# Kernel optimization log

Hardware: AMD Instinct MI355X
Metric: run time of the kernel (lower is better)

The kernel has to match this reference:

```python
import jax, jax.numpy as jnp
import numpy as np

NEG_INF_MASK = -10000.0


def setup_inputs() -> dict:
    key = jax.random.key(0)
    ks = jax.random.split(key, 6)
    B, S, D, H, K = 2, 2048, 1024, 16, 64
    return {
        "from_tensor": jax.random.normal(ks[0], (B, S, D), jnp.float32),
        "to_tensor": jax.random.normal(ks[1], (B, S, D), jnp.float32),
        "attention_mask": jax.random.randint(ks[2], (B, S), 0, 2, jnp.int32),
        "Wq": jax.random.normal(ks[3], (D, H, K), jnp.float32) * 0.02,
        "bq": jnp.zeros((H, K), jnp.float32),
        "Wk": jax.random.normal(ks[4], (D, H, K), jnp.float32) * 0.02,
        "bk": jnp.zeros((H, K), jnp.float32),
        "Wv": jax.random.normal(ks[5], (D, H, K), jnp.float32) * 0.02,
        "bv": jnp.zeros((H, K), jnp.float32),
    }


def reference(from_tensor, to_tensor, attention_mask, Wq, bq, Wk, bk, Wv, bv):
    # 3D dense projections: [B,S,D] x [D,H,K] -> [B,H,S,K] (transpose fused into einsum)
    q = jnp.einsum("bfd,dhk->bhfk", from_tensor, Wq) + bq[None, :, None, :]
    k = jnp.einsum("btd,dhk->bhtk", to_tensor, Wk) + bk[None, :, None, :]
    v = jnp.einsum("btd,dhk->bhtk", to_tensor, Wv) + bv[None, :, None, :]

    head_dim = q.shape[-1]
    logits = jnp.einsum("bhfk,bhtk->bhft", q, k) / jnp.sqrt(jnp.float32(head_dim))

    # key-padding mask: ones[B,1,F,1] @ mask[B,1,T,1]^T == broadcast mask over F
    mask = attention_mask.astype(jnp.float32)[:, None, None, :]  # [B,1,1,T]
    logits = logits + (1.0 - mask) * NEG_INF_MASK

    probs = jax.nn.softmax(logits, axis=-1)  # dropout prob = 0.0 -> no-op
    # context: [B,H,F,T] x [B,H,T,K] -> [B,F,H,K] (output transpose fused)
    return jnp.einsum("bhft,bhtk->bfhk", probs, v)
```

## Files before the change

kernel.cpp:

```cpp
#include <hip/hip_runtime.h>
#include <hip/hip_bf16.h>
#include <stdint.h>

#define B_   2
#define S_   2048
#define D_   1024
#define H_   16
#define KD_  64
#define TB   64

typedef __bf16 bf16_t;
typedef __bf16 bf16x8 __attribute__((ext_vector_type(8)));
typedef __bf16 bf16x4 __attribute__((ext_vector_type(4)));
typedef float  f32x4  __attribute__((ext_vector_type(4)));

#define MFMA16(A, B, C) __builtin_amdgcn_mfma_f32_16x16x32_bf16((A), (B), (C), 0, 0, 0)

__device__ __forceinline__ void gload_lds16(const void* g, void* l) {
    auto gp = (const __attribute__((address_space(1))) void*)(uintptr_t)(g);
    auto lp = (__attribute__((address_space(3))) void*)(uint32_t)(uintptr_t)(l);
    __builtin_amdgcn_global_load_lds(gp, lp, 16, 0, 0);
}

__global__ __launch_bounds__(256) void cvt_f32_bf16(const float* __restrict__ in,
                                                    bf16_t* __restrict__ out, int n4) {
    int idx = blockIdx.x * blockDim.x + threadIdx.x;
    int stride = gridDim.x * blockDim.x;
    for (int i = idx; i < n4; i += stride) {
        float4 v = ((const float4*)in)[i];
        bf16x4 o = {(bf16_t)v.x, (bf16_t)v.y, (bf16_t)v.z, (bf16_t)v.w};
        ((bf16x4*)out)[i] = o;
    }
}

__global__ __launch_bounds__(256) void transpose_w(const float* __restrict__ W,
                                                   bf16_t* __restrict__ Wt) {
    __shared__ float tile[32][33];
    const int tx = threadIdx.x & 31;
    const int ty = threadIdx.x >> 5;
    const int bx = blockIdx.x * 32;
    const int by = blockIdx.y * 32;
#pragma unroll
    for (int j = 0; j < 32; j += 8)
        tile[ty + j][tx] = W[(size_t)(by + ty + j) * D_ + bx + tx];
    __syncthreads();
#pragma unroll
    for (int j = 0; j < 32; j += 8)
        Wt[(size_t)(bx + ty + j) * D_ + by + tx] = (bf16_t)tile[tx][ty + j];
}

__global__ __launch_bounds__(256) void mask_k(const int* __restrict__ mask,
                                              float* __restrict__ madd, int n) {
    int i = blockIdx.x * blockDim.x + threadIdx.x;
    if (i < n) madd[i] = (1.0f - (float)mask[i]) * -10000.0f;
}

__global__ __launch_bounds__(512) void proj_gemm_fused(const bf16_t* __restrict__ Xf,
                                                       const bf16_t* __restrict__ Xt,
                                                       const bf16_t* __restrict__ Wt0,
                                                       const float* __restrict__ bq,
                                                       const float* __restrict__ bk,
                                                       const float* __restrict__ bv,
                                                       bf16_t* __restrict__ Qb,
                                                       bf16_t* __restrict__ Kb,
                                                       bf16_t* __restrict__ Vtb) {
    __shared__ bf16_t As[128 * 32];
    __shared__ bf16_t Bs[128 * 32];
    const int which = blockIdx.z;
    const bf16_t* X  = (which == 0) ? Xf : Xt;
    const bf16_t* Wt = Wt0 + (size_t)which * D_ * D_;
    const float* bias = (which == 0) ? bq : (which == 1) ? bk : bv;

    const int tid  = threadIdx.x;
    const int w    = tid >> 6;
    const int lane = tid & 63;
    const int wr   = w >> 2;
    const int wc   = w & 3;
    const int g    = lane >> 4;
    const int c    = lane & 15;
    const int m0 = blockIdx.y * 128;
    const int n0 = blockIdx.x * 128;

    f32x4 acc[4][2] = {};

    const int srow = w * 16 + (lane >> 2);
    const int scol = (lane & 3) * 8;
    const bf16_t* gA = X  + (size_t)(m0 + srow) * D_ + scol;
    const bf16_t* gB = Wt + (size_t)(n0 + srow) * D_ + scol;
    char* lA = (char*)As + w * 1024;
    char* lB = (char*)Bs + w * 1024;

    for (int k0 = 0; k0 < D_; k0 += 32) {
        __syncthreads();
        gload_lds16(gA + k0, lA);
        gload_lds16(gB + k0, lB);
        __syncthreads();

        bf16x8 af[4], bfr[2];
#pragma unroll
        for (int i = 0; i < 4; ++i)
            af[i] = *(const bf16x8*)&As[(wr * 64 + i * 16 + c) * 32 + g * 8];
#pragma unroll
        for (int j = 0; j < 2; ++j)
            bfr[j] = *(const bf16x8*)&Bs[(wc * 32 + j * 16 + c) * 32 + g * 8];
#pragma unroll
        for (int i = 0; i < 4; ++i)
#pragma unroll
            for (int j = 0; j < 2; ++j)
                acc[i][j] = MFMA16(af[i], bfr[j], acc[i][j]);
    }

#pragma unroll
    for (int i = 0; i < 4; ++i)
#pragma unroll
        for (int j = 0; j < 2; ++j)
#pragma unroll
            for (int r = 0; r < 4; ++r) {
                int m = m0 + wr * 64 + i * 16 + g * 4 + r;
                int n = n0 + wc * 32 + j * 16 + c;
                float val = acc[i][j][r] + bias[n];
                int b = m >> 11, s = m & 2047, hh = n >> 6, kd = n & 63;
                if (which == 0)
                    Qb[(size_t)(((b * H_ + hh) * S_ + s)) * KD_ + kd] = (bf16_t)(val * 0.125f);
                else if (which == 1)
                    Kb[(size_t)(((b * H_ + hh) * S_ + s)) * KD_ + kd] = (bf16_t)val;
                else
                    Vtb[(size_t)(((b * H_ + hh) * KD_ + kd)) * S_ + s] = (bf16_t)val;
            }
}

__global__ __launch_bounds__(256) void attn_kernel(const bf16_t* __restrict__ Q,
                                                   const bf16_t* __restrict__ K,
                                                   const bf16_t* __restrict__ Vt,
                                                   const float* __restrict__ maskadd,
                                                   float* __restrict__ out) {
    __shared__ __align__(16) bf16_t Ks[2][8 * 64 * 8];
    __shared__ __align__(16) bf16_t Vs[2][8 * 64 * 8];
    __shared__ __align__(16) float  Ms[S_];
    __shared__ __align__(16) bf16_t P_lds[4][32][88];
    const int tid = threadIdx.x;
    const int w = tid >> 6, lane = tid & 63;
    const int g = lane >> 4, c = lane & 15;
    const int b = blockIdx.z, h = blockIdx.y;
    const int qbase = blockIdx.x * 128 + w * 32;

    const bf16_t* Qp = Q + (size_t)(b * H_ + h) * S_ * KD_;
    const char* Kb8 = (const char*)(K + (size_t)(b * H_ + h) * S_ * KD_);
    const char* Vb8 = (const char*)(Vt + (size_t)(b * H_ + h) * KD_ * S_);
    const float* mp = maskadd + b * S_;

    {
        const float4* src = (const float4*)mp;
        float4* dst = (float4*)Ms;
        dst[tid] = src[tid];
        dst[tid + 256] = src[tid + 256];
    }

    bf16x8 qf[2][2];
#pragma unroll
    for (int qh = 0; qh < 2; ++qh) {
        qf[qh][0] = *(const bf16x8*)&Qp[(size_t)(qbase + qh * 16 + c) * KD_ + g * 8];
        qf[qh][1] = *(const bf16x8*)&Qp[(size_t)(qbase + qh * 16 + c) * KD_ + 32 + g * 8];
    }

    const char* srcK = Kb8 + lane * 128 + w * 16;
    const char* srcV = Vb8 + (size_t)lane * (S_ * 2) + w * 16;

    f32x4 o_acc[2][4] = {};
    float l_part[2][4] = {};

    {
        char* dK = (char*)Ks + w * 1024;
        char* dV = (char*)Vs + w * 1024;
        gload_lds16(srcK, dK);
        gload_lds16(srcK + 64, dK + 4096);
        gload_lds16(srcV, dV);
        gload_lds16(srcV + 64, dV + 4096);
    }
    __syncthreads();

    int buf = 0;
    for (int t0 = 0; t0 < S_; t0 += TB) {
        if (t0 + TB < S_) {
            char* dK = (char*)Ks + (buf ^ 1) * 8192 + w * 1024;
            char* dV = (char*)Vs + (buf ^ 1) * 8192 + w * 1024;
            gload_lds16(srcK + (t0 + TB) * 128,      dK);
            gload_lds16(srcK + (t0 + TB) * 128 + 64, dK + 4096);
            gload_lds16(srcV + (t0 + TB) * 2,        dV);
            gload_lds16(srcV + (t0 + TB) * 2 + 64,   dV + 4096);
        }
        const char* ksb = (const char*)Ks + buf * 8192;
        const char* vsb = (const char*)Vs + buf * 8192;

        f32x4 s[2][4];
#pragma unroll
        for (int tc = 0; tc < 4; ++tc) {
            const int row = tc * 16 + c;
            bf16x8 k0 = *(const bf16x8*)(ksb + g * 1024 + row * 16);
            bf16x8 k1 = *(const bf16x8*)(ksb + (4 + g) * 1024 + row * 16);
#pragma unroll
            for (int qh = 0; qh < 2; ++qh) {
                f32x4 z = {};
                z = MFMA16(qf[qh][0], k0, z);
                s[qh][tc] = MFMA16(qf[qh][1], k1, z);
            }
        }
#pragma unroll
        for (int tc = 0; tc < 4; ++tc) {
            float ma = Ms[t0 + tc * 16 + c];
#pragma unroll
            for (int qh = 0; qh < 2; ++qh)
#pragma unroll
                for (int r = 0; r < 4; ++r) s[qh][tc][r] += ma;
        }
#pragma unroll
        for (int qh = 0; qh < 2; ++qh) {
#pragma unroll
            for (int r = 0; r < 4; ++r) {
                float rs = 0.f;
#pragma unroll
                for (int tc = 0; tc < 4; ++tc) {
                    float p = __expf(s[qh][tc][r]);
                    s[qh][tc][r] = p;
                    rs += p;
                }
                l_part[qh][r] += rs;
            }
#pragma unroll
            for (int tc = 0; tc < 4; ++tc)
#pragma unroll
                for (int r = 0; r < 4; ++r)
                    P_lds[w][qh * 16 + g * 4 + r][tc * 16 + c] = (bf16_t)s[qh][tc][r];
        }
        bf16x8 pa[2][2];
#pragma unroll
        for (int qh = 0; qh < 2; ++qh) {
            pa[qh][0] = *(const bf16x8*)&P_lds[w][qh * 16 + c][g * 8];
            pa[qh][1] = *(const bf16x8*)&P_lds[w][qh * 16 + c][32 + g * 8];
        }
#pragma unroll
        for (int nc = 0; nc < 4; ++nc) {
            const int row = nc * 16 + c;
            bf16x8 v0 = *(const bf16x8*)(vsb + g * 1024 + row * 16);
            bf16x8 v1 = *(const bf16x8*)(vsb + (4 + g) * 1024 + row * 16);
#pragma unroll
            for (int qh = 0; qh < 2; ++qh) {
                o_acc[qh][nc] = MFMA16(pa[qh][0], v0, o_acc[qh][nc]);
                o_acc[qh][nc] = MFMA16(pa[qh][1], v1, o_acc[qh][nc]);
            }
        }
        __syncthreads();
        buf ^= 1;
    }
#pragma unroll
    for (int qh = 0; qh < 2; ++qh)
#pragma unroll
        for (int r = 0; r < 4; ++r) {
            float rs = l_part[qh][r];
            rs += __shfl_xor(rs, 1);
            rs += __shfl_xor(rs, 2);
            rs += __shfl_xor(rs, 4);
            rs += __shfl_xor(rs, 8);
            l_part[qh][r] = rs;
        }
#pragma unroll
    for (int qh = 0; qh < 2; ++qh)
#pragma unroll
        for (int nc = 0; nc < 4; ++nc)
#pragma unroll
            for (int r = 0; r < 4; ++r) {
                int qrow = qbase + qh * 16 + g * 4 + r;
                out[(size_t)((b * S_ + qrow) * H_ + h) * KD_ + nc * 16 + c] =
                    o_acc[qh][nc][r] / l_part[qh][r];
            }
}

extern "C" void kernel_launch(void* const* d_in, const int* in_sizes, int n_in,
                              void* d_out, int out_size, void* d_ws, size_t ws_size,
                              hipStream_t stream) {
    const float* from = (const float*)d_in[0];
    const float* to   = (const float*)d_in[1];
    const int*   amsk = (const int*)d_in[2];
    const float* Wq   = (const float*)d_in[3];
    const float* bq   = (const float*)d_in[4];
    const float* Wk   = (const float*)d_in[5];
    const float* bk   = (const float*)d_in[6];
    const float* Wv   = (const float*)d_in[7];
    const float* bv   = (const float*)d_in[8];
    float* out = (float*)d_out;
    char* ws = (char*)d_ws;

    const size_t SZ_X   = (size_t)(B_ * S_) * D_ * 2;
    const size_t SZ_W   = (size_t)D_ * D_ * 2;
    const size_t SZ_QKV = (size_t)B_ * H_ * S_ * KD_ * 2;
    size_t off = 0;
    bf16_t* Xf  = (bf16_t*)(ws + off); off += SZ_X;
    bf16_t* Xt  = (bf16_t*)(ws + off); off += SZ_X;
    bf16_t* Wtq = (bf16_t*)(ws + off); off += SZ_W;
    bf16_t* Wtk = (bf16_t*)(ws + off); off += SZ_W;
    bf16_t* Wtv = (bf16_t*)(ws + off); off += SZ_W;
    bf16_t* Qb  = (bf16_t*)(ws + off); off += SZ_QKV;
    bf16_t* Kb  = (bf16_t*)(ws + off); off += SZ_QKV;
    bf16_t* Vtb = (bf16_t*)(ws + off); off += SZ_QKV;
    float*  madd = (float*)(ws + off); off += (size_t)B_ * S_ * 4;

    const int n4 = (B_ * S_ * D_) / 4;
    cvt_f32_bf16<<<2048, 256, 0, stream>>>(from, Xf, n4);
    cvt_f32_bf16<<<2048, 256, 0, stream>>>(to,   Xt, n4);
    transpose_w<<<dim3(32, 32), 256, 0, stream>>>(Wq, Wtq);
    transpose_w<<<dim3(32, 32), 256, 0, stream>>>(Wk, Wtk);
    transpose_w<<<dim3(32, 32), 256, 0, stream>>>(Wv, Wtv);
    mask_k<<<(B_ * S_ + 255) / 256, 256, 0, stream>>>(amsk, madd, B_ * S_);

    proj_gemm_fused<<<dim3(D_ / 128, (B_ * S_) / 128, 3), 512, 0, stream>>>(
        Xf, Xt, Wtq, bq, bk, bv, Qb, Kb, Vtb);

    attn_kernel<<<dim3(S_ / 128, H_, B_), 256, 0, stream>>>(Qb, Kb, Vtb, madd, out);
}
```

Baseline: 208.0 us.

## Merge prep launches, fold mask into attention, double-buffer projection GEMM LDS

The two f32-to-bf16 conversions become one launch using grid z, and the three weight transposes become one launch. The separate mask kernel is removed and the additive mask is computed from the int mask directly inside the attention kernel's LDS fill. The projection GEMM now double-buffers its A/B LDS tiles, prefetching the next k-slice with global_load_lds while computing the current one, so one barrier per iteration is removed. This cuts launch overhead and aims to overlap load latency with MFMA work. The cost is twice the LDS in the GEMM. The prefetch is issued without an explicit wait before the barrier, so correctness relies on the barrier covering completion of the async LDS loads.

```diff
diff --git a/kernel.cpp b/kernel.cpp
--- a/kernel.cpp
+++ b/kernel.cpp
@@ -22,8 +22,12 @@
     __builtin_amdgcn_global_load_lds(gp, lp, 16, 0, 0);
 }
 
-__global__ __launch_bounds__(256) void cvt_f32_bf16(const float* __restrict__ in,
-                                                    bf16_t* __restrict__ out, int n4) {
+__global__ __launch_bounds__(256) void cvt_f32_bf16_2(const float* __restrict__ a,
+                                                      const float* __restrict__ bt,
+                                                      bf16_t* __restrict__ oa,
+                                                      bf16_t* __restrict__ ob, int n4) {
+    const float* in = blockIdx.z ? bt : a;
+    bf16_t* out = blockIdx.z ? ob : oa;
     int idx = blockIdx.x * blockDim.x + threadIdx.x;
     int stride = gridDim.x * blockDim.x;
     for (int i = idx; i < n4; i += stride) {
@@ -33,8 +37,13 @@
     }
 }
 
-__global__ __launch_bounds__(256) void transpose_w(const float* __restrict__ W,
-                                                   bf16_t* __restrict__ Wt) {
+__global__ __launch_bounds__(256) void transpose_w3(const float* __restrict__ Wq,
+                                                    const float* __restrict__ Wk,
+                                                    const float* __restrict__ Wv,
+                                                    bf16_t* __restrict__ Wt0) {
+    const int z = blockIdx.z;
+    const float* W = (z == 0) ? Wq : (z == 1) ? Wk : Wv;
+    bf16_t* Wt = Wt0 + (size_t)z * D_ * D_;
     __shared__ float tile[32][33];
     const int tx = threadIdx.x & 31;
     const int ty = threadIdx.x >> 5;
@@ -47,12 +56,6 @@
 #pragma unroll
     for (int j = 0; j < 32; j += 8)
         Wt[(size_t)(bx + ty + j) * D_ + by + tx] = (bf16_t)tile[tx][ty + j];
-}
-
-__global__ __launch_bounds__(256) void mask_k(const int* __restrict__ mask,
-                                              float* __restrict__ madd, int n) {
-    int i = blockIdx.x * blockDim.x + threadIdx.x;
-    if (i < n) madd[i] = (1.0f - (float)mask[i]) * -10000.0f;
 }
 
 __global__ __launch_bounds__(512) void proj_gemm_fused(const bf16_t* __restrict__ Xf,
@@ -64,8 +67,8 @@
                                                        bf16_t* __restrict__ Qb,
                                                        bf16_t* __restrict__ Kb,
                                                        bf16_t* __restrict__ Vtb) {
-    __shared__ bf16_t As[128 * 32];
-    __shared__ bf16_t Bs[128 * 32];
+    __shared__ bf16_t As[2][128 * 32];
+    __shared__ bf16_t Bs[2][128 * 32];
     const int which = blockIdx.z;
     const bf16_t* X  = (which == 0) ? Xf : Xt;
     const bf16_t* Wt = Wt0 + (size_t)which * D_ * D_;
@@ -87,27 +90,33 @@
     const int scol = (lane & 3) * 8;
     const bf16_t* gA = X  + (size_t)(m0 + srow) * D_ + scol;
     const bf16_t* gB = Wt + (size_t)(n0 + srow) * D_ + scol;
-    char* lA = (char*)As + w * 1024;
-    char* lB = (char*)Bs + w * 1024;
-
+
+    gload_lds16(gA, (char*)As[0] + w * 1024);
+    gload_lds16(gB, (char*)Bs[0] + w * 1024);
+    __syncthreads();
+
+    int buf = 0;
     for (int k0 = 0; k0 < D_; k0 += 32) {
-        __syncthreads();
-        gload_lds16(gA + k0, lA);
-        gload_lds16(gB + k0, lB);
-        __syncthreads();
+        if (k0 + 32 < D_) {
+            gload_lds16(gA + k0 + 32, (char*)As[buf ^ 1] + w * 1024);
+            gload_lds16(gB + k0 + 32, (char*)Bs[buf ^ 1] + w * 1024);
+        }
 
         bf16x8 af[4], bfr[2];
 #pragma unroll
         for (int i = 0; i < 4; ++i)
-            af[i] = *(const bf16x8*)&As[(wr * 64 + i * 16 + c) * 32 + g * 8];
+            af[i] = *(const bf16x8*)&As[buf][(wr * 64 + i * 16 + c) * 32 + g * 8];
 #pragma unroll
         for (int j = 0; j < 2; ++j)
-            bfr[j] = *(const bf16x8*)&Bs[(wc * 32 + j * 16 + c) * 32 + g * 8];
+            bfr[j] = *(const bf16x8*)&Bs[buf][(wc * 32 + j * 16 + c) * 32 + g * 8];
 #pragma unroll
         for (int i = 0; i < 4; ++i)
 #pragma unroll
             for (int j = 0; j < 2; ++j)
                 acc[i][j] = MFMA16(af[i], bfr[j], acc[i][j]);
+
+        __syncthreads();
+        buf ^= 1;
     }
 
 #pragma unroll
@@ -132,7 +141,7 @@
 __global__ __launch_bounds__(256) void attn_kernel(const bf16_t* __restrict__ Q,
                                                    const bf16_t* __restrict__ K,
                                                    const bf16_t* __restrict__ Vt,
-                                                   const float* __restrict__ maskadd,
+                                                   const int* __restrict__ amask,
                                                    float* __restrict__ out) {
     __shared__ __align__(16) bf16_t Ks[2][8 * 64 * 8];
     __shared__ __align__(16) bf16_t Vs[2][8 * 64 * 8];
@@ -147,13 +156,20 @@
     const bf16_t* Qp = Q + (size_t)(b * H_ + h) * S_ * KD_;
     const char* Kb8 = (const char*)(K + (size_t)(b * H_ + h) * S_ * KD_);
     const char* Vb8 = (const char*)(Vt + (size_t)(b * H_ + h) * KD_ * S_);
-    const float* mp = maskadd + b * S_;
+    const int* mp = amask + b * S_;
 
     {
-        const float4* src = (const float4*)mp;
-        float4* dst = (float4*)Ms;
-        dst[tid] = src[tid];
-        dst[tid + 256] = src[tid + 256];
+        const int4* src = (const int4*)mp;
+#pragma unroll
+        for (int half = 0; half < 2; ++half) {
+            int4 v = src[tid + half * 256];
+            float4 o;
+            o.x = (1.0f - (float)v.x) * -10000.0f;
+            o.y = (1.0f - (float)v.y) * -10000.0f;
+            o.z = (1.0f - (float)v.z) * -10000.0f;
+            o.w = (1.0f - (float)v.w) * -10000.0f;
+            ((float4*)Ms)[tid + half * 256] = o;
+        }
     }
 
     bf16x8 qf[2][2];
@@ -296,24 +312,17 @@
     size_t off = 0;
     bf16_t* Xf  = (bf16_t*)(ws + off); off += SZ_X;
     bf16_t* Xt  = (bf16_t*)(ws + off); off += SZ_X;
-    bf16_t* Wtq = (bf16_t*)(ws + off); off += SZ_W;
-    bf16_t* Wtk = (bf16_t*)(ws + off); off += SZ_W;
-    bf16_t* Wtv = (bf16_t*)(ws + off); off += SZ_W;
+    bf16_t* Wtq = (bf16_t*)(ws + off); off += 3 * SZ_W;
     bf16_t* Qb  = (bf16_t*)(ws + off); off += SZ_QKV;
     bf16_t* Kb  = (bf16_t*)(ws + off); off += SZ_QKV;
     bf16_t* Vtb = (bf16_t*)(ws + off); off += SZ_QKV;
-    float*  madd = (float*)(ws + off); off += (size_t)B_ * S_ * 4;
 
     const int n4 = (B_ * S_ * D_) / 4;
-    cvt_f32_bf16<<<2048, 256, 0, stream>>>(from, Xf, n4);
-    cvt_f32_bf16<<<2048, 256, 0, stream>>>(to,   Xt, n4);
-    transpose_w<<<dim3(32, 32), 256, 0, stream>>>(Wq, Wtq);
-    transpose_w<<<dim3(32, 32), 256, 0, stream>>>(Wk, Wtk);
-    transpose_w<<<dim3(32, 32), 256, 0, stream>>>(Wv, Wtv);
-    mask_k<<<(B_ * S_ + 255) / 256, 256, 0, stream>>>(amsk, madd, B_ * S_);
+    cvt_f32_bf16_2<<<dim3(2048, 1, 2), 256, 0, stream>>>(from, to, Xf, Xt, n4);
+    transpose_w3<<<dim3(32, 32, 3), 256, 0, stream>>>(Wq, Wk, Wv, Wtq);
 
     proj_gemm_fused<<<dim3(D_ / 128, (B_ * S_) / 128, 3), 512, 0, stream>>>(
         Xf, Xt, Wtq, bq, bk, bv, Qb, Kb, Vtb);
 
-    attn_kernel<<<dim3(S_ / 128, H_, B_), 256, 0, stream>>>(Qb, Kb, Vtb, madd, out);
-}
+    attn_kernel<<<dim3(S_ / 128, H_, B_), 256, 0, stream>>>(Qb, Kb, Vtb, amsk, out);
+}
```

Result: faster. 200.7 us (-3.5%).
